# Optimization experiments

Hardware: AMD Instinct MI355X
Metric: run time of the kernel (lower is better)

Reference implementation:

```python
import jax, jax.numpy as jnp
import numpy as np

B, T, C, K, NC = 256, 240, 512, 64, 4  # batch, chunk_size, dim, clusters, num_classes+1
EPS = 1e-12


def setup_inputs() -> dict:
    key = jax.random.key(0)
    k1, k2, k3, k4 = jax.random.split(key, 4)
    inputs = jax.random.normal(k1, (B, T, C), dtype=jnp.float32)
    conv_w = jax.random.normal(k2, (K, C), dtype=jnp.float32) * 0.05   # 1x1 assignment conv, no bias (vladv2=False)
    centroids = jax.random.normal(k3, (K, C), dtype=jnp.float32)
    fc_w = jax.random.normal(k4, (NC, K * C), dtype=jnp.float32) * 0.02
    fc_b = jnp.zeros((NC,), dtype=jnp.float32)
    return {"inputs": inputs, "conv_w": conv_w, "centroids": centroids, "fc_w": fc_w, "fc_b": fc_b}


def _l2norm(x, axis):
    return x / jnp.clip(jnp.linalg.norm(x, axis=axis, keepdims=True), EPS)


def reference(inputs, conv_w, centroids, fc_w, fc_b):
    # inputs: [B, T, C]. Torch permutes to NCHW=(B, C, T, 1); feature dim = C.
    x = _l2norm(inputs, axis=-1)                      # normalize_input over feature dim
    # soft assignment: 1x1 conv -> logits [B, T, K], softmax over clusters
    a = jax.nn.softmax(jnp.einsum('btc,kc->btk', x, conv_w), axis=-1)
    # vlad[b,k,c] = sum_t a[b,t,k] * (x[b,t,c] - centroids[k,c])
    #            = einsum(a, x) - (sum_t a) * centroids   (avoids [B,K,C,T] intermediate)
    vlad = jnp.einsum('btk,btc->bkc', a, x) - a.sum(axis=1)[:, :, None] * centroids[None]
    vlad = _l2norm(vlad, axis=-1)                     # intra-normalization over C
    v = vlad.reshape(vlad.shape[0], -1)               # [B, K*C]
    v = _l2norm(v, axis=-1)                           # final L2 normalize
    # dropout is identity in eval mode; fc + sigmoid
    return jax.nn.sigmoid(v @ fc_w.T + fc_b)
```

## Files before the change

kernel.cpp:

```cpp
#include <hip/hip_runtime.h>
#include <hip/hip_bf16.h>
#include <stdint.h>

#define BB 256
#define TT 240
#define CC 512
#define KK 64
#define NCLS 4
#define CHUNK 32
#define NCHUNK 8
#define THREADS 1024

#define CBS 72
#define TBS 2312
#define XELEMS (8 * TBS)

typedef __attribute__((ext_vector_type(8))) short bf16x8;
typedef __attribute__((ext_vector_type(4))) float f32x4;
typedef __attribute__((ext_vector_type(2))) unsigned int u32x2;

__device__ __forceinline__ unsigned short f2bf(float f) {
    union { float f; unsigned int i; } x; x.f = f;
    unsigned int r = x.i + 0x7FFFu + ((x.i >> 16) & 1u);
    return (unsigned short)(r >> 16);
}
__device__ __forceinline__ unsigned int pk2cvt(float lo, float hi) {
    union { __hip_bfloat162 h; unsigned int u; } c;
    c.h = __float22bfloat162_rn(float2{lo, hi});
    return c.u;
}
__device__ __forceinline__ void LB() {
    asm volatile("s_waitcnt lgkmcnt(0)\n\ts_barrier" ::: "memory");
}

struct alignas(16) SMemChunk {
    unsigned short x[2][XELEMS];
    float logitsP[2][CHUNK][67];
    unsigned short aT[KK][40];
    float sumsqP[CHUNK][68];
};
struct alignas(16) SMemEpi { unsigned short vbuf[KK * CC]; };
union SMemU { SMemChunk c; SMemEpi e; };

__global__ __launch_bounds__(THREADS, 4) void netvlad_kernel(
    const float* __restrict__ inp,
    const float* __restrict__ convw,
    const float* __restrict__ cent,
    const float* __restrict__ fcw,
    const float* __restrict__ fcb,
    float* __restrict__ out)
{
    __shared__ SMemU sm;
    __shared__ float asum[KK];
    __shared__ float ssred[4][KK];
    __shared__ float gred[16];
    __shared__ float fcred[16][NCLS];
    __shared__ float vinv_sh;

    const int tid  = threadIdx.x;
    const int b    = blockIdx.x;
    const int w    = tid >> 6;
    const int lane = tid & 63;
    const int grp  = (lane >> 4) & 3;
    const int col  = lane & 15;
    const int cg   = w & 3;
    const int th   = (w >> 2) & 1;
    const int kh   = w >> 3;
    const int cq   = w >> 2;

    if (tid < KK) asum[tid] = 0.f;

    f32x4 acc[8];
    #pragma unroll
    for (int j = 0; j < 8; ++j) acc[j] = (f32x4){0.f, 0.f, 0.f, 0.f};

    bf16x8 cw[8];
    #pragma unroll
    for (int s = 0; s < 8; ++s) {
        const float* p = convw + (size_t)(cg * 16 + col) * CC + (kh * 8 + s) * 32 + grp * 8;
        float4 a0 = *(const float4*)p;
        float4 a1 = *(const float4*)(p + 4);
        bf16x8 v;
        v[0] = (short)f2bf(a0.x); v[1] = (short)f2bf(a0.y);
        v[2] = (short)f2bf(a0.z); v[3] = (short)f2bf(a0.w);
        v[4] = (short)f2bf(a1.x); v[5] = (short)f2bf(a1.y);
        v[6] = (short)f2bf(a1.z); v[7] = (short)f2bf(a1.w);
        cw[s] = v;
    }

    const size_t ibase = (size_t)b * (TT * CC);

    float4 r0[2], r1[2];
    #pragma unroll
    for (int i = 0; i < 2; ++i) {
        int g = tid + i * THREADS;
        int t = g >> 6, c8 = (g & 63) << 3;
        const float* p = inp + ibase + (size_t)t * CC + c8;
        r0[i] = *(const float4*)p;
        r1[i] = *(const float4*)(p + 4);
    }

    for (int ch = 0; ch < NCHUNK; ++ch) {
        const int t0 = ch * CHUNK;
        const int tvalid = (TT - t0 < CHUNK) ? (TT - t0) : CHUNK;
        const int buf = ch & 1;
        unsigned short* xb = sm.c.x[buf];

        #pragma unroll
        for (int i = 0; i < 2; ++i) {
            int g = tid + i * THREADS;
            int t = g >> 6, c8 = (g & 63) << 3;
            float4 u0 = r0[i], u1 = r1[i];
            uint4 val = (uint4){pk2cvt(u0.x, u0.y), pk2cvt(u0.z, u0.w),
                                pk2cvt(u1.x, u1.y), pk2cvt(u1.z, u1.w)};
            float s = u0.x*u0.x + u0.y*u0.y + u0.z*u0.z + u0.w*u0.w
                    + u1.x*u1.x + u1.y*u1.y + u1.z*u1.z + u1.w*u1.w;
            if (t >= tvalid) { val = (uint4){0u,0u,0u,0u}; s = 0.f; }
            int off = (t >> 2) * TBS + (c8 >> 4) * CBS + (t & 3) * 16 + (c8 & 15);
            *(uint4*)&xb[off] = val;
            sm.c.sumsqP[t][lane] = s;
        }
        if (ch + 1 < NCHUNK) {
            int nt0 = t0 + CHUNK;
            #pragma unroll
            for (int i = 0; i < 2; ++i) {
                int g = tid + i * THREADS;
                int t = g >> 6, c8 = (g & 63) << 3;
                int gt = nt0 + t; if (gt > TT - 1) gt = TT - 1;
                const float* p = inp + ibase + (size_t)gt * CC + c8;
                r0[i] = *(const float4*)p;
                r1[i] = *(const float4*)(p + 4);
            }
        }
        LB();

        {
            f32x4 lt = (f32x4){0.f, 0.f, 0.f, 0.f};
            const int t = th * 16 + col;
            const int rb = (t >> 2) * TBS + (t & 3) * 16 + ((grp & 1) << 3);
            #pragma unroll
            for (int s = 0; s < 8; ++s) {
                const bf16x8 bb = *(const bf16x8*)&xb[rb + ((kh * 8 + s) * 2 + (grp >> 1)) * CBS];
                lt = __builtin_amdgcn_mfma_f32_16x16x32_bf16(cw[s], bb, lt, 0, 0, 0);
            }
            #pragma unroll
            for (int r = 0; r < 4; ++r)
                sm.c.logitsP[kh][t][cg * 16 + grp * 4 + r] = lt[r];
        }
        LB();

        if (tid < 512) {
            int t = tid >> 4, part = tid & 15;
            float4 sp = *(const float4*)&sm.c.sumsqP[t][part * 4];
            float ss = sp.x + sp.y + sp.z + sp.w;

            float l[4]; float lmax = -1e30f;
            #pragma unroll
            for (int q = 0; q < 4; ++q) {
                l[q] = sm.c.logitsP[0][t][q * 16 + part] +
                       sm.c.logitsP[1][t][q * 16 + part];
                lmax = fmaxf(lmax, l[q]);
            }
            #pragma unroll
            for (int m = 1; m < 16; m <<= 1) {
                lmax = fmaxf(lmax, __shfl_xor(lmax, m));
                ss  += __shfl_xor(ss, m);
            }
            float rinv = 1.f / fmaxf(sqrtf(ss), 1e-12f);
            rinv = (t < tvalid) ? rinv : 0.f;
            float m0 = lmax * rinv;
            float es = 0.f;
            #pragma unroll
            for (int q = 0; q < 4; ++q) { l[q] = __expf(l[q] * rinv - m0); es += l[q]; }
            #pragma unroll
            for (int m = 1; m < 16; m <<= 1) es += __shfl_xor(es, m);
            float is = 1.f / es;
            #pragma unroll
            for (int q = 0; q < 4; ++q) {
                float a = l[q] * is;
                sm.c.logitsP[0][t][q * 16 + part] = a;
                sm.c.aT[q * 16 + part][t] = (unsigned short)f2bf(a * rinv);
            }
        }
        LB();

        if (tid < KK) {
            float s = 0.f;
            for (int t = 0; t < tvalid; ++t) s += sm.c.logitsP[0][t][tid];
            asum[tid] += s;
        }
        {
            bf16x8 af = *(const bf16x8*)&sm.c.aT[cg * 16 + col][grp * 8];
            unsigned xvb = (unsigned)(uintptr_t)&xb[(grp * 2) * TBS + (cq * 8) * CBS + col];
            #pragma unroll
            for (int hh = 0; hh < 2; ++hh) {
                u32x2 lo[4], hi[4];
                #pragma unroll
                for (int j2 = 0; j2 < 4; ++j2) {
                    const unsigned o = (unsigned)((hh * 4 + j2) * 2 * CBS);
                    asm volatile("ds_read_b64_tr_b16 %0, %1"
                                 : "=v"(lo[j2]) : "v"(xvb + o));
                    asm volatile("ds_read_b64_tr_b16 %0, %1"
                                 : "=v"(hi[j2]) : "v"(xvb + o + (unsigned)(2 * TBS)));
                }
                asm volatile("s_waitcnt lgkmcnt(0)" ::: "memory");
                __builtin_amdgcn_sched_barrier(0);
                #pragma unroll
                for (int j2 = 0; j2 < 4; ++j2) {
                    union { bf16x8 v; u32x2 u[2]; } pk;
                    pk.u[0] = lo[j2]; pk.u[1] = hi[j2];
                    acc[hh * 4 + j2] = __builtin_amdgcn_mfma_f32_16x16x32_bf16(
                        af, pk.v, acc[hh * 4 + j2], 0, 0, 0);
                }
            }
        }
    }

    LB();

    #pragma unroll
    for (int r = 0; r < 4; ++r) {
        int cl = cg * 16 + grp * 4 + r;
        float as = asum[cl];
        float ss = 0.f;
        #pragma unroll
        for (int j = 0; j < 8; ++j) {
            int c = cq * 128 + j * 16 + col;
            float v = acc[j][r] - as * cent[(size_t)cl * CC + c];
            acc[j][r] = v;
            ss += v * v;
        }
        ss += __shfl_xor(ss, 1); ss += __shfl_xor(ss, 2);
        ss += __shfl_xor(ss, 4); ss += __shfl_xor(ss, 8);
        if (col == 0) ssred[cq][cl] = ss;
    }
    LB();

    float contrib = 0.f;
    #pragma unroll
    for (int r = 0; r < 4; ++r) {
        int cl = cg * 16 + grp * 4 + r;
        float ss = ssred[0][cl] + ssred[1][cl] + ssred[2][cl] + ssred[3][cl];
        float inv = 1.f / fmaxf(sqrtf(ss), 1e-12f);
        #pragma unroll
        for (int j = 0; j < 8; ++j) {
            float v = acc[j][r] * inv;
            acc[j][r] = v;
            contrib += v * v;
        }
    }
    #pragma unroll
    for (int m = 1; m < 64; m <<= 1) contrib += __shfl_xor(contrib, m);
    if (lane == 0) gred[w] = contrib;
    LB();
    if (tid == 0) {
        float tot = 0.f;
        #pragma unroll
        for (int i = 0; i < 16; ++i) tot += gred[i];
        vinv_sh = 1.f / fmaxf(sqrtf(tot), 1e-12f);
    }
    LB();

    {
        float vinv = vinv_sh;
        #pragma unroll
        for (int r = 0; r < 4; ++r) {
            int cl = cg * 16 + grp * 4 + r;
            #pragma unroll
            for (int j = 0; j < 8; ++j) {
                int c = cq * 128 + j * 16 + col;
                sm.e.vbuf[cl * CC + c] = f2bf(acc[j][r] * vinv);
            }
        }
    }
    LB();

    float pacc[NCLS] = {0.f, 0.f, 0.f, 0.f};
    #pragma unroll
    for (int i = 0; i < 4; ++i) {
        int idx = i * 8192 + tid * 8;
        bf16x8 vv = *(const bf16x8*)&sm.e.vbuf[idx];
        float vf[8];
        #pragma unroll
        for (int h = 0; h < 8; ++h) {
            union { unsigned int u; float f; } cvt;
            cvt.u = ((unsigned int)(unsigned short)vv[h]) << 16;
            vf[h] = cvt.f;
        }
        #pragma unroll
        for (int nc = 0; nc < NCLS; ++nc) {
            const float* wp = fcw + (size_t)nc * (KK * CC) + idx;
            float4 w0 = *(const float4*)wp;
            float4 w1 = *(const float4*)(wp + 4);
            pacc[nc] += vf[0] * w0.x + vf[1] * w0.y + vf[2] * w0.z + vf[3] * w0.w
                      + vf[4] * w1.x + vf[5] * w1.y + vf[6] * w1.z + vf[7] * w1.w;
        }
    }
    #pragma unroll
    for (int nc = 0; nc < NCLS; ++nc) {
        #pragma unroll
        for (int m = 1; m < 64; m <<= 1) pacc[nc] += __shfl_xor(pacc[nc], m);
    }
    if (lane == 0) {
        #pragma unroll
        for (int nc = 0; nc < NCLS; ++nc) fcred[w][nc] = pacc[nc];
    }
    LB();
    if (tid < NCLS) {
        float s = fcb[tid];
        #pragma unroll
        for (int ww = 0; ww < 16; ++ww) s += fcred[ww][tid];
        out[b * NCLS + tid] = 1.f / (1.f + __expf(-s));
    }
}

extern "C" void kernel_launch(void* const* d_in, const int* in_sizes, int n_in,
                              void* d_out, int out_size, void* d_ws, size_t ws_size,
                              hipStream_t stream) {
    const float* inp   = (const float*)d_in[0];
    const float* convw = (const float*)d_in[1];
    const float* cent  = (const float*)d_in[2];
    const float* fcw   = (const float*)d_in[3];
    const float* fcb   = (const float*)d_in[4];
    float* o = (float*)d_out;
    netvlad_kernel<<<BB, THREADS, 0, stream>>>(inp, convw, cent, fcw, fcb, o);
}
```

Before: 204.6 us.

## Split each batch over two blocks along time with workspace epilogue kernel

Splits the T dimension of each batch across two blocks (512 blocks total), processing 16-step chunks with a triple-buffered LDS staging scheme. Partial VLAD accumulators and assignment sums go to a global workspace, and a separate epilogue kernel combines them, subtracts centroids, normalizes and applies the FC layer. The goal is more parallelism and occupancy on a 256-block launch. The cost is a second kernel launch plus writing and re-reading 64x512 floats per half-batch. The old single-kernel path is kept as a fallback when the workspace is too small.

New measurement: 331.1 us. +61.9%, slower.

```diff
diff --git a/kernel.cpp b/kernel.cpp
--- a/kernel.cpp
+++ b/kernel.cpp
@@ -7,13 +7,13 @@
 #define CC 512
 #define KK 64
 #define NCLS 4
-#define CHUNK 32
-#define NCHUNK 8
 #define THREADS 1024
 
-#define CBS 72
-#define TBS 2312
-#define XELEMS (8 * TBS)
+#define THALF 120
+#define NCH1 8
+#define CBS 64
+#define TBS 2056
+#define XELEMS (4*TBS)
 
 typedef __attribute__((ext_vector_type(8))) short bf16x8;
 typedef __attribute__((ext_vector_type(4))) float f32x4;
@@ -33,24 +33,329 @@
     asm volatile("s_waitcnt lgkmcnt(0)\n\ts_barrier" ::: "memory");
 }
 
-struct alignas(16) SMemChunk {
-    unsigned short x[2][XELEMS];
+struct alignas(16) SMem1 {
+    unsigned short x[3][XELEMS];
+    float logitsP[4][16][67];
+    unsigned short aT[KK][40];
+    float sumsqP[2][16][16];
+    float asumP[4][KK];
+};
+
+__device__ __forceinline__ void stage_chunk(SMem1* sm, float4 u0, float4 u1,
+        int t_s, int c8, int lane, int tv, int buf, int sbuf) {
+    uint4 val = (uint4){pk2cvt(u0.x, u0.y), pk2cvt(u0.z, u0.w),
+                        pk2cvt(u1.x, u1.y), pk2cvt(u1.z, u1.w)};
+    float s = u0.x*u0.x + u0.y*u0.y + u0.z*u0.z + u0.w*u0.w
+            + u1.x*u1.x + u1.y*u1.y + u1.z*u1.z + u1.w*u1.w;
+    if (t_s >= tv) { val = (uint4){0u,0u,0u,0u}; s = 0.f; }
+    int off = (t_s >> 2) * TBS + (c8 >> 4) * CBS + (t_s & 3) * 16 + (c8 & 15);
+    *(uint4*)&sm->x[buf][off] = val;
+    s += __shfl_xor(s, 16); s += __shfl_xor(s, 32);
+    if (lane < 16) sm->sumsqP[sbuf][t_s][lane] = s;
+}
+
+__global__ __launch_bounds__(THREADS, 8) void netvlad_main(
+    const float* __restrict__ inp,
+    const float* __restrict__ convw,
+    float* __restrict__ wsv,
+    float* __restrict__ wsa)
+{
+    __shared__ SMem1 sm;
+
+    const int tid  = threadIdx.x;
+    const int blk  = blockIdx.x;
+    const int b    = blk >> 1;
+    const int half = blk & 1;
+    const int w    = tid >> 6;
+    const int lane = tid & 63;
+    const int grp  = (lane >> 4) & 3;
+    const int col  = lane & 15;
+    const int cg   = w & 3;
+    const int kh   = w >> 2;
+    const int cq   = w >> 2;
+
+    if (tid < 256) ((float*)sm.asumP)[tid] = 0.f;
+
+    f32x4 acc[8];
+    #pragma unroll
+    for (int j = 0; j < 8; ++j) acc[j] = (f32x4){0.f, 0.f, 0.f, 0.f};
+
+    bf16x8 cw[4];
+    #pragma unroll
+    for (int s = 0; s < 4; ++s) {
+        const float* p = convw + (size_t)(cg * 16 + col) * CC + (kh * 4 + s) * 32 + grp * 8;
+        float4 a0 = *(const float4*)p;
+        float4 a1 = *(const float4*)(p + 4);
+        bf16x8 v;
+        v[0] = (short)f2bf(a0.x); v[1] = (short)f2bf(a0.y);
+        v[2] = (short)f2bf(a0.z); v[3] = (short)f2bf(a0.w);
+        v[4] = (short)f2bf(a1.x); v[5] = (short)f2bf(a1.y);
+        v[6] = (short)f2bf(a1.z); v[7] = (short)f2bf(a1.w);
+        cw[s] = v;
+    }
+
+    const size_t ibase = (size_t)b * (TT * CC);
+    const int tbase = half * THALF;
+    const int t_s = tid >> 6;
+    const int c8  = lane << 3;
+
+    float4 r0, r1;
+    {
+        int tg = tbase + t_s;
+        const float* p = inp + ibase + (size_t)tg * CC + c8;
+        float4 u0 = *(const float4*)p, u1 = *(const float4*)(p + 4);
+        stage_chunk(&sm, u0, u1, t_s, c8, lane, 16, 0, 0);
+    }
+    {
+        int tg = tbase + 16 + t_s;
+        const float* p = inp + ibase + (size_t)tg * CC + c8;
+        r0 = *(const float4*)p; r1 = *(const float4*)(p + 4);
+    }
+    LB();
+
+    int bufc = 0, bufp = 2;
+    for (int ch = 0; ch < NCH1; ++ch) {
+        int bufn = bufc + 1; if (bufn == 3) bufn = 0;
+        const int tv = (THALF - ch * 16 > 16) ? 16 : (THALF - ch * 16);
+
+        if (ch + 1 < NCH1) {
+            int tvn = THALF - (ch + 1) * 16; if (tvn > 16) tvn = 16;
+            stage_chunk(&sm, r0, r1, t_s, c8, lane, tvn, bufn, (ch + 1) & 1);
+        }
+        if (ch + 2 < NCH1) {
+            int tg = tbase + (ch + 2) * 16 + t_s; if (tg > TT - 1) tg = TT - 1;
+            const float* p = inp + ibase + (size_t)tg * CC + c8;
+            r0 = *(const float4*)p; r1 = *(const float4*)(p + 4);
+        }
+
+        {
+            const unsigned short* xb = sm.x[bufc];
+            f32x4 lt = (f32x4){0.f, 0.f, 0.f, 0.f};
+            const int rb = (col >> 2) * TBS + (col & 3) * 16 + (grp & 1) * 8;
+            #pragma unroll
+            for (int s = 0; s < 4; ++s) {
+                int cb = (kh * 4 + s) * 2 + (grp >> 1);
+                bf16x8 bb = *(const bf16x8*)&xb[rb + cb * CBS];
+                lt = __builtin_amdgcn_mfma_f32_16x16x32_bf16(cw[s], bb, lt, 0, 0, 0);
+            }
+            #pragma unroll
+            for (int r = 0; r < 4; ++r)
+                sm.logitsP[kh][col][cg * 16 + grp * 4 + r] = lt[r];
+        }
+        LB();
+
+        if (tid < 256) {
+            int t = tid >> 4, part = tid & 15;
+            float ss = sm.sumsqP[ch & 1][t][part];
+            float l[4]; float lmax = -1e30f;
+            #pragma unroll
+            for (int q = 0; q < 4; ++q) {
+                int c = q * 16 + part;
+                l[q] = sm.logitsP[0][t][c] + sm.logitsP[1][t][c]
+                     + sm.logitsP[2][t][c] + sm.logitsP[3][t][c];
+                lmax = fmaxf(lmax, l[q]);
+            }
+            #pragma unroll
+            for (int m = 1; m < 16; m <<= 1) {
+                lmax = fmaxf(lmax, __shfl_xor(lmax, m));
+                ss  += __shfl_xor(ss, m);
+            }
+            float rinv = 1.f / fmaxf(sqrtf(ss), 1e-12f);
+            rinv = (t < tv) ? rinv : 0.f;
+            float m0 = lmax * rinv;
+            float es = 0.f;
+            #pragma unroll
+            for (int q = 0; q < 4; ++q) { l[q] = __expf(l[q] * rinv - m0); es += l[q]; }
+            #pragma unroll
+            for (int m = 1; m < 16; m <<= 1) es += __shfl_xor(es, m);
+            float is = 1.f / es;
+            int tofs = (ch & 1) * 16;
+            float am[4];
+            #pragma unroll
+            for (int q = 0; q < 4; ++q) {
+                float a = l[q] * is;
+                sm.aT[q * 16 + part][tofs + t] = (unsigned short)f2bf(a * rinv);
+                am[q] = (t < tv) ? a : 0.f;
+            }
+            #pragma unroll
+            for (int q = 0; q < 4; ++q) { am[q] += __shfl_xor(am[q], 16); am[q] += __shfl_xor(am[q], 32); }
+            if (lane < 16) {
+                #pragma unroll
+                for (int q = 0; q < 4; ++q) sm.asumP[w][q * 16 + lane] += am[q];
+            }
+        }
+        LB();
+
+        if (ch & 1) {
+            bf16x8 af = *(const bf16x8*)&sm.aT[cg * 16 + col][grp * 8];
+            unsigned bsel = (grp >> 1) ? (unsigned)bufc : (unsigned)bufp;
+            unsigned base = (unsigned)(uintptr_t)&sm.x[0][0]
+                + (bsel * (unsigned)XELEMS
+                   + (unsigned)(((grp & 1) * 2) * TBS + (cq * 8) * CBS + col)) * 2u;
+            #pragma unroll
+            for (int hh = 0; hh < 2; ++hh) {
+                u32x2 lo[4], hi[4];
+                #pragma unroll
+                for (int j2 = 0; j2 < 4; ++j2) {
+                    unsigned o = base + (unsigned)((hh * 4 + j2) * (2 * CBS));
+                    asm volatile("ds_read_b64_tr_b16 %0, %1" : "=v"(lo[j2]) : "v"(o));
+                    asm volatile("ds_read_b64_tr_b16 %0, %1" : "=v"(hi[j2]) : "v"(o + (unsigned)(2 * TBS)));
+                }
+                asm volatile("s_waitcnt lgkmcnt(0)" ::: "memory");
+                __builtin_amdgcn_sched_barrier(0);
+                #pragma unroll
+                for (int j2 = 0; j2 < 4; ++j2) {
+                    union { bf16x8 v; u32x2 u[2]; } pk;
+                    pk.u[0] = lo[j2]; pk.u[1] = hi[j2];
+                    acc[hh * 4 + j2] = __builtin_amdgcn_mfma_f32_16x16x32_bf16(
+                        af, pk.v, acc[hh * 4 + j2], 0, 0, 0);
+                }
+            }
+            LB();
+        }
+        bufp = bufc; bufc = bufn;
+    }
+
+    if (tid < KK) {
+        float a = sm.asumP[0][tid] + sm.asumP[1][tid] + sm.asumP[2][tid] + sm.asumP[3][tid];
+        wsa[blk * KK + tid] = a;
+    }
+    float* wv = wsv + (size_t)blk * (KK * CC);
+    #pragma unroll
+    for (int r = 0; r < 4; ++r) {
+        int cl = cg * 16 + grp * 4 + r;
+        #pragma unroll
+        for (int j = 0; j < 8; ++j)
+            wv[cl * CC + cq * 128 + j * 16 + col] = acc[j][r];
+    }
+}
+
+struct alignas(16) SMem2 {
+    unsigned short vbuf[KK][520];
+    float gred[16];
+    float fcred[16][NCLS];
+    float vinv;
+};
+
+__global__ __launch_bounds__(THREADS) void netvlad_epi(
+    const float* __restrict__ wsv, const float* __restrict__ wsa,
+    const float* __restrict__ cent, const float* __restrict__ fcw,
+    const float* __restrict__ fcb, float* __restrict__ out)
+{
+    __shared__ SMem2 sm;
+    const int tid = threadIdx.x, b = blockIdx.x;
+    const int w = tid >> 6, lane = tid & 63;
+    const int cl = tid >> 4, part = tid & 15, c0 = part * 32;
+
+    const float* v0 = wsv + (size_t)(2 * b) * (KK * CC) + (size_t)cl * CC + c0;
+    const float* v1 = v0 + KK * CC;
+    const float* cp = cent + (size_t)cl * CC + c0;
+    float as = wsa[(2 * b) * KK + cl] + wsa[(2 * b + 1) * KK + cl];
+
+    float v[32]; float ss = 0.f;
+    #pragma unroll
+    for (int i = 0; i < 8; ++i) {
+        float4 a  = *(const float4*)(v0 + 4 * i);
+        float4 bq = *(const float4*)(v1 + 4 * i);
+        float4 c4 = *(const float4*)(cp + 4 * i);
+        float x0 = a.x + bq.x - as * c4.x;
+        float x1 = a.y + bq.y - as * c4.y;
+        float x2 = a.z + bq.z - as * c4.z;
+        float x3 = a.w + bq.w - as * c4.w;
+        v[4*i] = x0; v[4*i+1] = x1; v[4*i+2] = x2; v[4*i+3] = x3;
+        ss += x0*x0 + x1*x1 + x2*x2 + x3*x3;
+    }
+    #pragma unroll
+    for (int m = 1; m < 16; m <<= 1) ss += __shfl_xor(ss, m);
+    float inv = 1.f / fmaxf(sqrtf(ss), 1e-12f);
+    float contrib = 0.f;
+    #pragma unroll
+    for (int i = 0; i < 32; ++i) { v[i] *= inv; contrib += v[i] * v[i]; }
+    #pragma unroll
+    for (int m = 1; m < 64; m <<= 1) contrib += __shfl_xor(contrib, m);
+    if (lane == 0) sm.gred[w] = contrib;
+    __syncthreads();
+    if (tid == 0) {
+        float tot = 0.f;
+        #pragma unroll
+        for (int i = 0; i < 16; ++i) tot += sm.gred[i];
+        sm.vinv = 1.f / fmaxf(sqrtf(tot), 1e-12f);
+    }
+    __syncthreads();
+    {
+        float vinv = sm.vinv;
+        #pragma unroll
+        for (int i = 0; i < 4; ++i) {
+            uint4 pv = (uint4){ pk2cvt(v[8*i]*vinv,   v[8*i+1]*vinv),
+                                pk2cvt(v[8*i+2]*vinv, v[8*i+3]*vinv),
+                                pk2cvt(v[8*i+4]*vinv, v[8*i+5]*vinv),
+                                pk2cvt(v[8*i+6]*vinv, v[8*i+7]*vinv) };
+            *(uint4*)&sm.vbuf[cl][c0 + 8 * i] = pv;
+        }
+    }
+    __syncthreads();
+
+    float pacc[NCLS] = {0.f, 0.f, 0.f, 0.f};
+    #pragma unroll
+    for (int i = 0; i < 4; ++i) {
+        int idx = i * 8192 + tid * 8;
+        int row = idx >> 9, off = idx & 511;
+        bf16x8 vv = *(const bf16x8*)&sm.vbuf[row][off];
+        float vf[8];
+        #pragma unroll
+        for (int h = 0; h < 8; ++h) {
+            union { unsigned int u; float f; } cvt;
+            cvt.u = ((unsigned int)(unsigned short)vv[h]) << 16;
+            vf[h] = cvt.f;
+        }
+        #pragma unroll
+        for (int nc = 0; nc < NCLS; ++nc) {
+            const float* wp = fcw + (size_t)nc * (KK * CC) + idx;
+            float4 w0 = *(const float4*)wp;
+            float4 w1 = *(const float4*)(wp + 4);
+            pacc[nc] += vf[0]*w0.x + vf[1]*w0.y + vf[2]*w0.z + vf[3]*w0.w
+                      + vf[4]*w1.x + vf[5]*w1.y + vf[6]*w1.z + vf[7]*w1.w;
+        }
+    }
+    #pragma unroll
+    for (int nc = 0; nc < NCLS; ++nc) {
+        #pragma unroll
+        for (int m = 1; m < 64; m <<= 1) pacc[nc] += __shfl_xor(pacc[nc], m);
+    }
+    if (lane == 0) {
+        #pragma unroll
+        for (int nc = 0; nc < NCLS; ++nc) sm.fcred[w][nc] = pacc[nc];
+    }
+    __syncthreads();
+    if (tid < NCLS) {
+        float s = fcb[tid];
+        #pragma unroll
+        for (int ww = 0; ww < 16; ++ww) s += sm.fcred[ww][tid];
+        out[b * NCLS + tid] = 1.f / (1.f + __expf(-s));
+    }
+}
+
+#define CHUNK 32
+#define NCHUNK 8
+#define FCBS 72
+#define FTBS 2312
+#define FXELEMS (8 * FTBS)
+
+struct alignas(16) SMemChunkF {
+    unsigned short x[2][FXELEMS];
     float logitsP[2][CHUNK][67];
     unsigned short aT[KK][40];
     float sumsqP[CHUNK][68];
 };
-struct alignas(16) SMemEpi { unsigned short vbuf[KK * CC]; };
-union SMemU { SMemChunk c; SMemEpi e; };
-
-__global__ __launch_bounds__(THREADS, 4) void netvlad_kernel(
-    const float* __restrict__ inp,
-    const float* __restrict__ convw,
-    const float* __restrict__ cent,
-    const float* __restrict__ fcw,
-    const float* __restrict__ fcb,
-    float* __restrict__ out)
+struct alignas(16) SMemEpiF { unsigned short vbuf[KK * CC]; };
+union SMemUF { SMemChunkF c; SMemEpiF e; };
+
+__global__ __launch_bounds__(THREADS, 4) void netvlad_fallback(
+    const float* __restrict__ inp, const float* __restrict__ convw,
+    const float* __restrict__ cent, const float* __restrict__ fcw,
+    const float* __restrict__ fcb, float* __restrict__ out)
 {
-    __shared__ SMemU sm;
+    __shared__ SMemUF sm;
     __shared__ float asum[KK];
     __shared__ float ssred[4][KK];
     __shared__ float gred[16];
@@ -116,7 +421,7 @@
             float s = u0.x*u0.x + u0.y*u0.y + u0.z*u0.z + u0.w*u0.w
                     + u1.x*u1.x + u1.y*u1.y + u1.z*u1.z + u1.w*u1.w;
             if (t >= tvalid) { val = (uint4){0u,0u,0u,0u}; s = 0.f; }
-            int off = (t >> 2) * TBS + (c8 >> 4) * CBS + (t & 3) * 16 + (c8 & 15);
+            int off = (t >> 2) * FTBS + (c8 >> 4) * FCBS + (t & 3) * 16 + (c8 & 15);
             *(uint4*)&xb[off] = val;
             sm.c.sumsqP[t][lane] = s;
         }
@@ -137,10 +442,10 @@
         {
             f32x4 lt = (f32x4){0.f, 0.f, 0.f, 0.f};
             const int t = th * 16 + col;
-            const int rb = (t >> 2) * TBS + (t & 3) * 16 + ((grp & 1) << 3);
+            const int rb = (t >> 2) * FTBS + (t & 3) * 16 + ((grp & 1) << 3);
             #pragma unroll
             for (int s = 0; s < 8; ++s) {
-                const bf16x8 bb = *(const bf16x8*)&xb[rb + ((kh * 8 + s) * 2 + (grp >> 1)) * CBS];
+                const bf16x8 bb = *(const bf16x8*)&xb[rb + ((kh * 8 + s) * 2 + (grp >> 1)) * FCBS];
                 lt = __builtin_amdgcn_mfma_f32_16x16x32_bf16(cw[s], bb, lt, 0, 0, 0);
             }
             #pragma unroll
@@ -153,7 +458,6 @@
             int t = tid >> 4, part = tid & 15;
             float4 sp = *(const float4*)&sm.c.sumsqP[t][part * 4];
             float ss = sp.x + sp.y + sp.z + sp.w;
-
             float l[4]; float lmax = -1e30f;
             #pragma unroll
             for (int q = 0; q < 4; ++q) {
@@ -191,17 +495,15 @@
         }
         {
             bf16x8 af = *(const bf16x8*)&sm.c.aT[cg * 16 + col][grp * 8];
-            unsigned xvb = (unsigned)(uintptr_t)&xb[(grp * 2) * TBS + (cq * 8) * CBS + col];
+            unsigned xvb = (unsigned)(uintptr_t)&xb[(grp * 2) * FTBS + (cq * 8) * FCBS + col];
             #pragma unroll
             for (int hh = 0; hh < 2; ++hh) {
                 u32x2 lo[4], hi[4];
                 #pragma unroll
                 for (int j2 = 0; j2 < 4; ++j2) {
-                    const unsigned o = (unsigned)((hh * 4 + j2) * 2 * CBS);
-                    asm volatile("ds_read_b64_tr_b16 %0, %1"
-                                 : "=v"(lo[j2]) : "v"(xvb + o));
-                    asm volatile("ds_read_b64_tr_b16 %0, %1"
-                                 : "=v"(hi[j2]) : "v"(xvb + o + (unsigned)(2 * TBS)));
+                    const unsigned o = (unsigned)((hh * 4 + j2) * 2 * FCBS);
+                    asm volatile("ds_read_b64_tr_b16 %0, %1" : "=v"(lo[j2]) : "v"(xvb + o));
+                    asm volatile("ds_read_b64_tr_b16 %0, %1" : "=v"(hi[j2]) : "v"(xvb + o + (unsigned)(2 * FTBS)));
                 }
                 asm volatile("s_waitcnt lgkmcnt(0)" ::: "memory");
                 __builtin_amdgcn_sched_barrier(0);
@@ -217,7 +519,6 @@
     }
 
     LB();
-
     #pragma unroll
     for (int r = 0; r < 4; ++r) {
         int cl = cg * 16 + grp * 4 + r;
@@ -235,7 +536,6 @@
         if (col == 0) ssred[cq][cl] = ss;
     }
     LB();
-
     float contrib = 0.f;
     #pragma unroll
     for (int r = 0; r < 4; ++r) {
@@ -260,7 +560,6 @@
         vinv_sh = 1.f / fmaxf(sqrtf(tot), 1e-12f);
     }
     LB();
-
     {
         float vinv = vinv_sh;
         #pragma unroll
@@ -274,7 +573,6 @@
         }
     }
     LB();
-
     float pacc[NCLS] = {0.f, 0.f, 0.f, 0.f};
     #pragma unroll
     for (int i = 0; i < 4; ++i) {
@@ -323,5 +621,14 @@
     const float* fcw   = (const float*)d_in[3];
     const float* fcb   = (const float*)d_in[4];
     float* o = (float*)d_out;
-    netvlad_kernel<<<BB, THREADS, 0, stream>>>(inp, convw, cent, fcw, fcb, o);
-}
+
+    const size_t need = (size_t)512 * KK * CC * 4 + (size_t)512 * KK * 4;
+    if (d_ws != nullptr && ws_size >= need) {
+        float* wsv = (float*)d_ws;
+        float* wsa = wsv + (size_t)512 * KK * CC;
+        netvlad_main<<<2 * BB, THREADS, 0, stream>>>(inp, convw, wsv, wsa);
+        netvlad_epi<<<BB, THREADS, 0, stream>>>(wsv, wsa, cent, fcw, fcb, o);
+    } else {
+        netvlad_fallback<<<BB, THREADS, 0, stream>>>(inp, convw, cent, fcw, fcb, o);
+    }
+}
```

## Software-pipeline chunk loop with triple-buffered x and deferred aggregation MFMA

Applied to the files above, without the earlier changes.

Restructures the per-chunk loop so x is triple-buffered in LDS and global loads are issued two chunks ahead. The aggregation MFMA for chunk ch-1 now runs in the same phase as the logits and softmax for chunk ch, which cuts the barriers per chunk from three to two. The softmax is spread across all 1024 threads (32 lanes per row), and the per-cluster assignment sums become per-wave partials reduced at the end. This trades more LDS and register use (a third x buffer, two prefetch register sets) for less barrier stalling and better overlap.

New measurement: 230.7 us. 1.13x slower.

```diff
diff --git a/kernel.cpp b/kernel.cpp
--- a/kernel.cpp
+++ b/kernel.cpp
@@ -8,7 +8,7 @@
 #define KK 64
 #define NCLS 4
 #define CHUNK 32
-#define NCHUNK 8
+#define NCH 8
 #define THREADS 1024
 
 #define CBS 72
@@ -34,13 +34,27 @@
 }
 
 struct alignas(16) SMemChunk {
-    unsigned short x[2][XELEMS];
+    unsigned short x[3][XELEMS];
     float logitsP[2][CHUNK][67];
-    unsigned short aT[KK][40];
-    float sumsqP[CHUNK][68];
+    unsigned short aT[2][KK][40];
+    float sumsqP[2][CHUNK][16];
+    float asumP[16][KK];
 };
 struct alignas(16) SMemEpi { unsigned short vbuf[KK * CC]; };
 union SMemU { SMemChunk c; SMemEpi e; };
+
+__device__ __forceinline__ void stage_row(unsigned short* xb, float* ssp,
+        float4 u0, float4 u1, int t, int c8, int lane, int tv) {
+    uint4 val = (uint4){pk2cvt(u0.x, u0.y), pk2cvt(u0.z, u0.w),
+                        pk2cvt(u1.x, u1.y), pk2cvt(u1.z, u1.w)};
+    float s = u0.x*u0.x + u0.y*u0.y + u0.z*u0.z + u0.w*u0.w
+            + u1.x*u1.x + u1.y*u1.y + u1.z*u1.z + u1.w*u1.w;
+    if (t >= tv) { val = (uint4){0u,0u,0u,0u}; s = 0.f; }
+    int off = (t >> 2) * TBS + (c8 >> 4) * CBS + (t & 3) * 16 + (c8 & 15);
+    *(uint4*)&xb[off] = val;
+    s += __shfl_xor(s, 16); s += __shfl_xor(s, 32);
+    if (lane < 16) ssp[t * 16 + lane] = s;
+}
 
 __global__ __launch_bounds__(THREADS, 4) void netvlad_kernel(
     const float* __restrict__ inp,
@@ -51,7 +65,7 @@
     float* __restrict__ out)
 {
     __shared__ SMemU sm;
-    __shared__ float asum[KK];
+    __shared__ float asumF[KK];
     __shared__ float ssred[4][KK];
     __shared__ float gred[16];
     __shared__ float fcred[16][NCLS];
@@ -68,11 +82,34 @@
     const int kh   = w >> 3;
     const int cq   = w >> 2;
 
-    if (tid < KK) asum[tid] = 0.f;
+    ((float*)sm.c.asumP)[tid] = 0.f;
 
     f32x4 acc[8];
     #pragma unroll
     for (int j = 0; j < 8; ++j) acc[j] = (f32x4){0.f, 0.f, 0.f, 0.f};
+
+    const size_t ibase = (size_t)b * (TT * CC);
+    const int c8 = lane << 3;
+
+#define ISSUE(pr, nc) do { \
+        int tg0_ = (nc) * CHUNK + w;      if (tg0_ > TT - 1) tg0_ = TT - 1; \
+        int tg1_ = (nc) * CHUNK + w + 16; if (tg1_ > TT - 1) tg1_ = TT - 1; \
+        const float* p0_ = inp + ibase + (size_t)tg0_ * CC + c8; \
+        const float* p1_ = inp + ibase + (size_t)tg1_ * CC + c8; \
+        pr[0] = *(const float4*)p0_; pr[1] = *(const float4*)(p0_ + 4); \
+        pr[2] = *(const float4*)p1_; pr[3] = *(const float4*)(p1_ + 4); \
+    } while (0)
+
+#define STAGE(pr, nc) do { \
+        const int tv_ = (TT - (nc) * CHUNK < CHUNK) ? (TT - (nc) * CHUNK) : CHUNK; \
+        unsigned short* xb_ = sm.c.x[(nc) % 3]; \
+        float* ssp_ = &sm.c.sumsqP[(nc) & 1][0][0]; \
+        stage_row(xb_, ssp_, pr[0], pr[1], w,      c8, lane, tv_); \
+        stage_row(xb_, ssp_, pr[2], pr[3], w + 16, c8, lane, tv_); \
+    } while (0)
+
+    float4 preA[4], preB[4];
+    ISSUE(preB, 0);
 
     bf16x8 cw[8];
     #pragma unroll
@@ -88,53 +125,18 @@
         cw[s] = v;
     }
 
-    const size_t ibase = (size_t)b * (TT * CC);
-
-    float4 r0[2], r1[2];
-    #pragma unroll
-    for (int i = 0; i < 2; ++i) {
-        int g = tid + i * THREADS;
-        int t = g >> 6, c8 = (g & 63) << 3;
-        const float* p = inp + ibase + (size_t)t * CC + c8;
-        r0[i] = *(const float4*)p;
-        r1[i] = *(const float4*)(p + 4);
-    }
-
-    for (int ch = 0; ch < NCHUNK; ++ch) {
-        const int t0 = ch * CHUNK;
-        const int tvalid = (TT - t0 < CHUNK) ? (TT - t0) : CHUNK;
-        const int buf = ch & 1;
-        unsigned short* xb = sm.c.x[buf];
-
-        #pragma unroll
-        for (int i = 0; i < 2; ++i) {
-            int g = tid + i * THREADS;
-            int t = g >> 6, c8 = (g & 63) << 3;
-            float4 u0 = r0[i], u1 = r1[i];
-            uint4 val = (uint4){pk2cvt(u0.x, u0.y), pk2cvt(u0.z, u0.w),
-                                pk2cvt(u1.x, u1.y), pk2cvt(u1.z, u1.w)};
-            float s = u0.x*u0.x + u0.y*u0.y + u0.z*u0.z + u0.w*u0.w
-                    + u1.x*u1.x + u1.y*u1.y + u1.z*u1.z + u1.w*u1.w;
-            if (t >= tvalid) { val = (uint4){0u,0u,0u,0u}; s = 0.f; }
-            int off = (t >> 2) * TBS + (c8 >> 4) * CBS + (t & 3) * 16 + (c8 & 15);
-            *(uint4*)&xb[off] = val;
-            sm.c.sumsqP[t][lane] = s;
-        }
-        if (ch + 1 < NCHUNK) {
-            int nt0 = t0 + CHUNK;
-            #pragma unroll
-            for (int i = 0; i < 2; ++i) {
-                int g = tid + i * THREADS;
-                int t = g >> 6, c8 = (g & 63) << 3;
-                int gt = nt0 + t; if (gt > TT - 1) gt = TT - 1;
-                const float* p = inp + ibase + (size_t)gt * CC + c8;
-                r0[i] = *(const float4*)p;
-                r1[i] = *(const float4*)(p + 4);
-            }
-        }
-        LB();
-
+    STAGE(preB, 0);
+    ISSUE(preA, 1);
+    ISSUE(preB, 2);
+    LB();
+
+    for (int ch = 0; ch < NCH; ++ch) {
+        if (ch + 1 < NCH) {
+            if (((ch + 1) & 1) == 1) STAGE(preA, ch + 1);
+            else                     STAGE(preB, ch + 1);
+        }
         {
+            const unsigned short* xb = sm.c.x[ch % 3];
             f32x4 lt = (f32x4){0.f, 0.f, 0.f, 0.f};
             const int t = th * 16 + col;
             const int rb = (t >> 2) * TBS + (t & 3) * 16 + ((grp & 1) << 3);
@@ -149,59 +151,57 @@
         }
         LB();
 
-        if (tid < 512) {
-            int t = tid >> 4, part = tid & 15;
-            float4 sp = *(const float4*)&sm.c.sumsqP[t][part * 4];
-            float ss = sp.x + sp.y + sp.z + sp.w;
-
-            float l[4]; float lmax = -1e30f;
-            #pragma unroll
-            for (int q = 0; q < 4; ++q) {
-                l[q] = sm.c.logitsP[0][t][q * 16 + part] +
-                       sm.c.logitsP[1][t][q * 16 + part];
-                lmax = fmaxf(lmax, l[q]);
-            }
-            #pragma unroll
-            for (int m = 1; m < 16; m <<= 1) {
+        if (ch + 3 < NCH) {
+            if (((ch + 3) & 1) == 1) ISSUE(preA, ch + 3);
+            else                     ISSUE(preB, ch + 3);
+        }
+        {
+            const int tv = (TT - ch * CHUNK < CHUNK) ? (TT - ch * CHUNK) : CHUNK;
+            const int t = tid >> 5;
+            const int p32 = lane & 31;
+            float ss = (p32 < 16) ? sm.c.sumsqP[ch & 1][t][p32] : 0.f;
+            float l0 = sm.c.logitsP[0][t][p32]      + sm.c.logitsP[1][t][p32];
+            float l1 = sm.c.logitsP[0][t][32 + p32] + sm.c.logitsP[1][t][32 + p32];
+            float lmax = fmaxf(l0, l1);
+            #pragma unroll
+            for (int m = 1; m < 32; m <<= 1) {
                 lmax = fmaxf(lmax, __shfl_xor(lmax, m));
                 ss  += __shfl_xor(ss, m);
             }
             float rinv = 1.f / fmaxf(sqrtf(ss), 1e-12f);
-            rinv = (t < tvalid) ? rinv : 0.f;
+            rinv = (t < tv) ? rinv : 0.f;
             float m0 = lmax * rinv;
-            float es = 0.f;
-            #pragma unroll
-            for (int q = 0; q < 4; ++q) { l[q] = __expf(l[q] * rinv - m0); es += l[q]; }
-            #pragma unroll
-            for (int m = 1; m < 16; m <<= 1) es += __shfl_xor(es, m);
+            l0 = __expf(l0 * rinv - m0);
+            l1 = __expf(l1 * rinv - m0);
+            float es = l0 + l1;
+            #pragma unroll
+            for (int m = 1; m < 32; m <<= 1) es += __shfl_xor(es, m);
             float is = 1.f / es;
-            #pragma unroll
-            for (int q = 0; q < 4; ++q) {
-                float a = l[q] * is;
-                sm.c.logitsP[0][t][q * 16 + part] = a;
-                sm.c.aT[q * 16 + part][t] = (unsigned short)f2bf(a * rinv);
-            }
-        }
-        LB();
-
-        if (tid < KK) {
-            float s = 0.f;
-            for (int t = 0; t < tvalid; ++t) s += sm.c.logitsP[0][t][tid];
-            asum[tid] += s;
-        }
-        {
-            bf16x8 af = *(const bf16x8*)&sm.c.aT[cg * 16 + col][grp * 8];
-            unsigned xvb = (unsigned)(uintptr_t)&xb[(grp * 2) * TBS + (cq * 8) * CBS + col];
+            float a0 = l0 * is, a1 = l1 * is;
+            sm.c.aT[ch & 1][p32][t]      = (unsigned short)f2bf(a0 * rinv);
+            sm.c.aT[ch & 1][32 + p32][t] = (unsigned short)f2bf(a1 * rinv);
+            float am0 = (t < tv) ? a0 : 0.f;
+            float am1 = (t < tv) ? a1 : 0.f;
+            am0 += __shfl_xor(am0, 32);
+            am1 += __shfl_xor(am1, 32);
+            if (lane < 32) {
+                sm.c.asumP[w][p32]      += am0;
+                sm.c.asumP[w][32 + p32] += am1;
+            }
+        }
+        if (ch >= 1) {
+            const int pc = ch - 1;
+            bf16x8 af = *(const bf16x8*)&sm.c.aT[pc & 1][cg * 16 + col][grp * 8];
+            unsigned xvb = (unsigned)(uintptr_t)
+                &sm.c.x[pc % 3][(grp * 2) * TBS + (cq * 8) * CBS + col];
             #pragma unroll
             for (int hh = 0; hh < 2; ++hh) {
                 u32x2 lo[4], hi[4];
                 #pragma unroll
                 for (int j2 = 0; j2 < 4; ++j2) {
                     const unsigned o = (unsigned)((hh * 4 + j2) * 2 * CBS);
-                    asm volatile("ds_read_b64_tr_b16 %0, %1"
-                                 : "=v"(lo[j2]) : "v"(xvb + o));
-                    asm volatile("ds_read_b64_tr_b16 %0, %1"
-                                 : "=v"(hi[j2]) : "v"(xvb + o + (unsigned)(2 * TBS)));
+                    asm volatile("ds_read_b64_tr_b16 %0, %1" : "=v"(lo[j2]) : "v"(xvb + o));
+                    asm volatile("ds_read_b64_tr_b16 %0, %1" : "=v"(hi[j2]) : "v"(xvb + o + (unsigned)(2 * TBS)));
                 }
                 asm volatile("s_waitcnt lgkmcnt(0)" ::: "memory");
                 __builtin_amdgcn_sched_barrier(0);
@@ -214,14 +214,46 @@
                 }
             }
         }
-    }
-
+        LB();
+    }
+
+    {
+        const int pc = NCH - 1;
+        bf16x8 af = *(const bf16x8*)&sm.c.aT[pc & 1][cg * 16 + col][grp * 8];
+        unsigned xvb = (unsigned)(uintptr_t)
+            &sm.c.x[pc % 3][(grp * 2) * TBS + (cq * 8) * CBS + col];
+        #pragma unroll
+        for (int hh = 0; hh < 2; ++hh) {
+            u32x2 lo[4], hi[4];
+            #pragma unroll
+            for (int j2 = 0; j2 < 4; ++j2) {
+                const unsigned o = (unsigned)((hh * 4 + j2) * 2 * CBS);
+                asm volatile("ds_read_b64_tr_b16 %0, %1" : "=v"(lo[j2]) : "v"(xvb + o));
+                asm volatile("ds_read_b64_tr_b16 %0, %1" : "=v"(hi[j2]) : "v"(xvb + o + (unsigned)(2 * TBS)));
+            }
+            asm volatile("s_waitcnt lgkmcnt(0)" ::: "memory");
+            __builtin_amdgcn_sched_barrier(0);
+            #pragma unroll
+            for (int j2 = 0; j2 < 4; ++j2) {
+                union { bf16x8 v; u32x2 u[2]; } pk;
+                pk.u[0] = lo[j2]; pk.u[1] = hi[j2];
+                acc[hh * 4 + j2] = __builtin_amdgcn_mfma_f32_16x16x32_bf16(
+                    af, pk.v, acc[hh * 4 + j2], 0, 0, 0);
+            }
+        }
+    }
+    if (tid < KK) {
+        float a = 0.f;
+        #pragma unroll
+        for (int ww = 0; ww < 16; ++ww) a += sm.c.asumP[ww][tid];
+        asumF[tid] = a;
+    }
     LB();
 
     #pragma unroll
     for (int r = 0; r < 4; ++r) {
         int cl = cg * 16 + grp * 4 + r;
-        float as = asum[cl];
+        float as = asumF[cl];
         float ss = 0.f;
         #pragma unroll
         for (int j = 0; j < 8; ++j) {
@@ -312,6 +344,8 @@
         for (int ww = 0; ww < 16; ++ww) s += fcred[ww][tid];
         out[b * NCLS + tid] = 1.f / (1.f + __expf(-s));
     }
+#undef ISSUE
+#undef STAGE
 }
 
 extern "C" void kernel_launch(void* const* d_in, const int* in_sizes, int n_in,
```
